# Kernel optimization log

Hardware: AMD Instinct MI355X
Metric: run time of the kernel (lower is better)

## Reference

```python
import jax, jax.numpy as jnp
import numpy as np

HEADS = 8
RANK = 4

def _lora(x, w_down, w_up, palette, in_dim, out_dim):
    # w_down: [RANK*in_dim, 15], w_up: [RANK*out_dim, 15], palette: [1, 15]
    down = (palette @ w_down.T).reshape(RANK, in_dim)   # [r, in]
    up = (palette @ w_up.T).reshape(out_dim, RANK)      # [out, r]
    return (x @ down.T) @ up.T                          # [..., out]


def setup_inputs() -> dict:
    key = jax.random.key(0)
    ks = jax.random.split(key, 16)
    B, S, D = 2, 2048, 1280
    def n(k, shape, std=0.02):
        return (jax.random.normal(k, shape, dtype=jnp.float32) * std).astype(jnp.float32)
    return {
        'hidden_states': jax.random.normal(ks[0], (B, S, D), dtype=jnp.float32),
        'color_palette': jax.random.uniform(ks[1], (1, 15), dtype=jnp.float32),
        'Wq': n(ks[2], (D, D)), 'Wk': n(ks[3], (D, D)),
        'Wv': n(ks[4], (D, D)), 'Wo': n(ks[5], (D, D)),
        'bo': jnp.zeros((D,), dtype=jnp.float32),
        'q_down': n(ks[6], (RANK * D, 15), 0.25), 'q_up': n(ks[7], (RANK * D, 15)),
        'k_down': n(ks[8], (RANK * D, 15), 0.25), 'k_up': n(ks[9], (RANK * D, 15)),
        'v_down': n(ks[10], (RANK * D, 15), 0.25), 'v_up': n(ks[11], (RANK * D, 15)),
        'o_down': n(ks[12], (RANK * D, 15), 0.25), 'o_up': n(ks[13], (RANK * D, 15)),
    }


def reference(hidden_states, color_palette, Wq, Wk, Wv, Wo, bo,
              q_down, q_up, k_down, k_up, v_down, v_up, o_down, o_up):
    B, S, D = hidden_states.shape
    H = HEADS
    hd = D // H
    scale = 1.0  # LoRA scale
    x = hidden_states
    # LoRA-augmented projections (self-attention: encoder_hidden_states = x)
    q = x @ Wq.T + scale * _lora(x, q_down, q_up, color_palette, D, D)
    k = x @ Wk.T + scale * _lora(x, k_down, k_up, color_palette, D, D)
    v = x @ Wv.T + scale * _lora(x, v_down, v_up, color_palette, D, D)
    # split heads: [B, S, D] -> [B, H, S, hd]
    q = q.reshape(B, S, H, hd).transpose(0, 2, 1, 3)
    k = k.reshape(B, S, H, hd).transpose(0, 2, 1, 3)
    v = v.reshape(B, S, H, hd).transpose(0, 2, 1, 3)
    attn_scale = 1.0 / jnp.sqrt(jnp.asarray(hd, dtype=q.dtype))
    scores = jnp.einsum('bhqd,bhkd->bhqk', q, k) * attn_scale
    probs = jax.nn.softmax(scores, axis=-1)
    out = jnp.einsum('bhqk,bhkd->bhqd', probs, v)
    out = out.transpose(0, 2, 1, 3).reshape(B, S, D)
    out = out @ Wo.T + bo + scale * _lora(out, o_down, o_up, color_palette, D, D)
    return out
```

## Files before the change

### kernel.cpp

```cpp
#include <hip/hip_runtime.h>

typedef unsigned short u16;
typedef unsigned int u32;
typedef __attribute__((ext_vector_type(4))) float floatx4;
typedef __attribute__((ext_vector_type(16))) float floatx16;
typedef __attribute__((ext_vector_type(8))) __bf16 bf16x8;
typedef __attribute__((ext_vector_type(2))) unsigned int u32x2;
typedef __attribute__((ext_vector_type(4))) unsigned int u32x4;

#define MFMA_BF16(a, b, c) __builtin_amdgcn_mfma_f32_16x16x32_bf16((a), (b), (c), 0, 0, 0)
#define MFMA32(a, b, c) __builtin_amdgcn_mfma_f32_32x32x16_bf16((a), (b), (c), 0, 0, 0)

typedef const __attribute__((address_space(1))) void* gas_ptr;
typedef __attribute__((address_space(3))) void* las_ptr;

__device__ __forceinline__ void gll16(const void* g, void* l) {
  __builtin_amdgcn_global_load_lds((gas_ptr)g, (las_ptr)l, 16, 0, 0);
}

__device__ __forceinline__ u16 f2bf(float x) {
  u32 u = __builtin_bit_cast(u32, x);
  u = (u + 0x7fffu + ((u >> 16) & 1u)) >> 16;
  return (u16)u;
}

__device__ __forceinline__ u32 cvtpk(float lo, float hi) {
  u32 r;
  asm("v_cvt_pk_bf16_f32 %0, %1, %2" : "=v"(r) : "v"(lo), "v"(hi));
  return r;
}

template <int WN>
__device__ __forceinline__ void vwait() {
  if constexpr (WN == 6) asm volatile("s_waitcnt vmcnt(6)" ::: "memory");
  else if constexpr (WN == 4) asm volatile("s_waitcnt vmcnt(4)" ::: "memory");
}

__global__ void prep_downup(const float* __restrict__ pal,
                            const float* __restrict__ qd, const float* __restrict__ qu,
                            const float* __restrict__ kd, const float* __restrict__ ku,
                            const float* __restrict__ vd, const float* __restrict__ vu,
                            const float* __restrict__ od, const float* __restrict__ ou,
                            float* __restrict__ down_f, float* __restrict__ up_f) {
  int tid = blockIdx.x * blockDim.x + threadIdx.x;
  int w = tid / 10240;
  int rem = tid - w * 10240;
  const float* dsrc = (w == 0) ? qd : (w == 1) ? kd : (w == 2) ? vd : od;
  const float* usrc = (w == 0) ? qu : (w == 1) ? ku : (w == 2) ? vu : ou;
  bool isdown = rem < 5120;
  int row = isdown ? rem : rem - 5120;
  const float* src = (isdown ? dsrc : usrc) + row * 15;
  float s = 0.f;
#pragma unroll
  for (int p = 0; p < 15; ++p) s += pal[p] * src[p];
  if (isdown) down_f[w * 5120 + row] = s;
  else        up_f[w * 5120 + row] = s;
}

__global__ void build_weff(const float* __restrict__ Wq, const float* __restrict__ Wk,
                           const float* __restrict__ Wv, const float* __restrict__ Wo,
                           const float* __restrict__ down_f, const float* __restrict__ up_f,
                           u16* __restrict__ weff_qkv, u16* __restrict__ weff_o) {
  int tid = blockIdx.x * blockDim.x + threadIdx.x;
  int w = tid / 1638400;
  int rem = tid - w * 1638400;
  int n = rem / 1280;
  int k = rem - n * 1280;
  const float* W = (w == 0) ? Wq : (w == 1) ? Wk : (w == 2) ? Wv : Wo;
  const float* up = up_f + w * 5120 + n * 4;
  const float* dn = down_f + w * 5120 + k;
  float v = W[rem] + up[0] * dn[0] + up[1] * dn[1280] + up[2] * dn[2560] + up[3] * dn[3840];
  u16 hv = f2bf(v);
  if (w < 3) weff_qkv[w * 1638400 + rem] = hv;
  else       weff_o[rem] = hv;
}

__global__ void cvt_x(const float4* __restrict__ x, ushort4* __restrict__ xb) {
  int i = blockIdx.x * blockDim.x + threadIdx.x;
  float4 v = x[i];
  ushort4 o;
  o.x = f2bf(v.x); o.y = f2bf(v.y); o.z = f2bf(v.z); o.w = f2bf(v.w);
  xb[i] = o;
}

__global__ __launch_bounds__(512) void gemm256_qkv(const u16* __restrict__ A, const u16* __restrict__ Bm,
                                                   u16* __restrict__ qb, u16* __restrict__ kb,
                                                   u16* __restrict__ vbuf, int K) {
  __shared__ __align__(16) u16 lA[2][16384];
  __shared__ __align__(16) u16 lB[2][16384];
  const int t = threadIdx.x;
  const int lane = t & 63;
  const int l15 = lane & 15, quad = lane >> 4;
  const int wid = t >> 6;
  const int wm = wid >> 2;
  const int wn = wid & 3;
  const int l = blockIdx.y * 16 + blockIdx.x;
  const int v = (l & 7) * 30 + (l >> 3);
  const int bm = (v & 15) * 256;
  const int bn = (v >> 4) * 256;
  floatx4 acc[8][4] = {};

  const int r0 = t >> 3, pos = t & 7;
  const long sof0 = (long)r0 * K + ((pos + r0) & 7) * 8;
  const long sof1 = (long)(r0 + 64) * K + ((pos + r0 + 64) & 7) * 8;

  int afo[4][2], bfo[2][2];
#pragma unroll
  for (int ch = 0; ch < 2; ++ch) {
    int kc8 = ch * 4 + quad;
#pragma unroll
    for (int mi = 0; mi < 4; ++mi) {
      int ra = wm * 128 + mi * 16 + l15;
      afo[mi][ch] = ra * 64 + ((kc8 - ra) & 7) * 8;
    }
#pragma unroll
    for (int ni = 0; ni < 2; ++ni) {
      int rb = wn * 64 + ni * 16 + l15;
      bfo[ni][ch] = rb * 64 + ((kc8 - rb) & 7) * 8;
    }
  }

  const u16* Ab = A + (long)bm * K;
  const u16* Bb = Bm + (long)bn * K;

#define PHASE(CB, Q, SB, SMAT, SH, ST, WN)                                           \
  {                                                                                   \
    const u16* gsrc = (SMAT) ? Bb : Ab;                                               \
    u16* ld0 = ((SMAT) ? &lB[SB][0] : &lA[SB][0]) + ((SH) * 1024 + t) * 8;            \
    gll16(gsrc + sof0 + (long)(SH) * 128 * K + (long)(ST) * 64, ld0);                 \
    gll16(gsrc + sof1 + (long)(SH) * 128 * K + (long)(ST) * 64, ld0 + 4096);          \
    vwait<WN>();                                                                      \
    __builtin_amdgcn_s_barrier();                                                     \
    __builtin_amdgcn_sched_barrier(0);                                                \
    constexpr int mh = (Q) >> 1, nh = (Q) & 1;                                        \
    bf16x8 af[4][2], bfr[2][2];                                                       \
    _Pragma("unroll") for (int ch = 0; ch < 2; ++ch) {                                \
      _Pragma("unroll") for (int mi = 0; mi < 4; ++mi)                                \
        af[mi][ch] = *(const bf16x8*)(&lA[CB][0] + afo[mi][ch] + mh * 4096);          \
      _Pragma("unroll") for (int ni = 0; ni < 2; ++ni)                                \
        bfr[ni][ch] = *(const bf16x8*)(&lB[CB][0] + bfo[ni][ch] + nh * 2048);         \
    }                                                                                 \
    asm volatile("s_waitcnt lgkmcnt(0)" ::: "memory");                                \
    __builtin_amdgcn_sched_barrier(0);                                                \
    __builtin_amdgcn_s_setprio(1);                                                    \
    _Pragma("unroll") for (int ch = 0; ch < 2; ++ch)                                  \
      _Pragma("unroll") for (int mi = 0; mi < 4; ++mi)                                \
        _Pragma("unroll") for (int ni = 0; ni < 2; ++ni)                              \
          acc[mh * 4 + mi][nh * 2 + ni] =                                             \
              MFMA_BF16(af[mi][ch], bfr[ni][ch], acc[mh * 4 + mi][nh * 2 + ni]);      \
    __builtin_amdgcn_s_setprio(0);                                                    \
  }

  gll16(Ab + sof0, &lA[0][t * 8]);
  gll16(Ab + sof1, &lA[0][t * 8 + 4096]);
  gll16(Bb + sof0, &lB[0][t * 8]);
  gll16(Bb + sof1, &lB[0][t * 8 + 4096]);
  gll16(Ab + sof0 + 128L * K, &lA[0][(1024 + t) * 8]);
  gll16(Ab + sof1 + 128L * K, &lA[0][(1024 + t) * 8 + 4096]);
  gll16(Bb + sof0 + 128L * K, &lB[0][(1024 + t) * 8]);
  gll16(Bb + sof1 + 128L * K, &lB[0][(1024 + t) * 8 + 4096]);

  const int niter = K >> 7;
  for (int i = 0; i < niter; ++i) {
    const int t1 = 2 * i + 1, t2 = 2 * i + 2;
    PHASE(0, 0, 1, 0, 0, t1, 6);
    PHASE(0, 1, 1, 1, 0, t1, 4);
    PHASE(0, 2, 1, 0, 1, t1, 0);
    PHASE(0, 3, 1, 1, 1, t1, 0);
    PHASE(1, 0, 0, 0, 0, t2, 6);
    PHASE(1, 1, 0, 1, 0, t2, 4);
    PHASE(1, 2, 0, 0, 1, t2, 0);
    PHASE(1, 3, 0, 1, 1, t2, 0);
  }
#undef PHASE
  asm volatile("s_waitcnt vmcnt(0)" ::: "memory");

#pragma unroll
  for (int mi8 = 0; mi8 < 8; ++mi8) {
#pragma unroll
    for (int ni4 = 0; ni4 < 4; ++ni4) {
#pragma unroll
      for (int r = 0; r < 4; ++r) {
        int m = bm + wm * 128 + (mi8 >> 2) * 64 + (mi8 & 3) * 16 + quad * 4 + r;
        int n = bn + wn * 64 + (ni4 >> 1) * 32 + (ni4 & 1) * 16 + l15;
        u16 hv = f2bf(acc[mi8][ni4][r]);
        if (n < 1280) {
          qb[(long)m * 1280 + n] = hv;
        } else if (n < 2560) {
          kb[(long)m * 1280 + (n - 1280)] = hv;
        } else {
          vbuf[(long)m * 1280 + (n - 2560)] = hv;
        }
      }
    }
  }
}

__global__ __launch_bounds__(256) void vtrans(const u16* __restrict__ vbuf,
                                              u16* __restrict__ vtb) {
  __shared__ u16 tile[64 * 65];
  const int t = threadIdx.x;
  const int sb = blockIdx.x * 64, nb = blockIdx.y * 64, b = blockIdx.z;
  const u16* src = vbuf + ((long)(b * 2048 + sb)) * 1280 + nb;
#pragma unroll
  for (int it = 0; it < 16; ++it) {
    int idx = t + it * 256;
    int s = idx >> 6, n = idx & 63;
    tile[s * 65 + n] = src[(long)s * 1280 + n];
  }
  __syncthreads();
  u16* dst = vtb + ((long)(b * 1280 + nb)) * 2048 + sb;
#pragma unroll
  for (int it = 0; it < 16; ++it) {
    int idx = t + it * 256;
    int n = idx >> 6, s = idx & 63;
    dst[(long)n * 2048 + s] = tile[s * 65 + n];
  }
}

__global__ __launch_bounds__(256) void gemm128_o(const u16* __restrict__ A, const u16* __restrict__ Bm,
                                                 float* __restrict__ outf,
                                                 const float* __restrict__ bias, int K) {
  __shared__ __align__(16) u16 lA[128 * 64];
  __shared__ __align__(16) u16 lB[128 * 64];
  const int t = threadIdx.x;
  const int lane = t & 63;
  const int l15 = lane & 15, quad = lane >> 4;
  const int wid = t >> 6;
  const int wm = (wid >> 1) * 64;
  const int wn = (wid & 1) * 64;
  const int bm = blockIdx.x * 128;
  const int bn = blockIdx.y * 128;
  floatx4 acc[4][4] = {};

  int soff[4];
#pragma unroll
  for (int i = 0; i < 4; ++i) {
    int c = t + i * 256;
    int row = c >> 3, pos = c & 7;
    soff[i] = row * K + ((pos + row) & 7) * 8;
  }
  int afo[4][2], bfo[4][2];
#pragma unroll
  for (int i = 0; i < 4; ++i) {
#pragma unroll
    for (int ch = 0; ch < 2; ++ch) {
      int ra = wm + i * 16 + l15;
      int rb = wn + i * 16 + l15;
      int kc8 = ch * 4 + quad;
      afo[i][ch] = ra * 64 + ((kc8 - ra) & 7) * 8;
      bfo[i][ch] = rb * 64 + ((kc8 - rb) & 7) * 8;
    }
  }

  const u16* Ab = A + (long)bm * K;
  const u16* Bb = Bm + (long)bn * K;
  const int nkt = K >> 6;

  for (int kt = 0; kt < nkt; ++kt) {
    __syncthreads();
    const int k0 = kt * 64;
#pragma unroll
    for (int i = 0; i < 4; ++i) gll16(Ab + (long)soff[i] + k0, lA + (t + i * 256) * 8);
#pragma unroll
    for (int i = 0; i < 4; ++i) gll16(Bb + (long)soff[i] + k0, lB + (t + i * 256) * 8);
    __syncthreads();
#pragma unroll
    for (int ch = 0; ch < 2; ++ch) {
      bf16x8 af[4], bfr[4];
#pragma unroll
      for (int i = 0; i < 4; ++i) af[i] = *(const bf16x8*)(lA + afo[i][ch]);
#pragma unroll
      for (int i = 0; i < 4; ++i) bfr[i] = *(const bf16x8*)(lB + bfo[i][ch]);
#pragma unroll
      for (int i = 0; i < 4; ++i)
#pragma unroll
        for (int j = 0; j < 4; ++j)
          acc[i][j] = MFMA_BF16(af[i], bfr[j], acc[i][j]);
    }
  }

#pragma unroll
  for (int i = 0; i < 4; ++i) {
#pragma unroll
    for (int j = 0; j < 4; ++j) {
#pragma unroll
      for (int r = 0; r < 4; ++r) {
        int m = bm + wm + i * 16 + quad * 4 + r;
        int n = bn + wn + j * 16 + l15;
        outf[(long)m * 1280 + n] = acc[i][j][r] + bias[n];
      }
    }
  }
}

__global__ __launch_bounds__(512) void flash_attn(const u16* __restrict__ qb,
                                                  const u16* __restrict__ kb,
                                                  const u16* __restrict__ vtb,
                                                  u16* __restrict__ attn) {
  const int D = 1280, HD = 160;
  __shared__ __align__(16) u16 kv_lds[2][20480];
  const int t = threadIdx.x, lane = t & 63, wid = t >> 6;
  const int l31 = lane & 31, hi = lane >> 5;
  const int rg = wid >> 1, kh = wid & 1;
  const int lflat = blockIdx.y * 16 + blockIdx.x;
  const int vswz = (lflat & 7) * 32 + (lflat >> 3);
  const int qi = vswz & 15, bh = vswz >> 4;
  const int b = bh >> 3, h = bh & 7;
  const int q0 = qi * 128 + rg * 32;
  const float kS = 0.11404582025f;

  bf16x8 aq[10];
  {
    const u16* qg = qb + ((long)(b * 2048 + q0 + l31)) * D + h * HD + hi * 8;
#pragma unroll
    for (int kw = 0; kw < 10; ++kw) aq[kw] = *(const bf16x8*)(qg + kw * 16);
  }

  const u16* sg[5];
  int sadv[5];
#pragma unroll
  for (int i = 0; i < 5; ++i) {
    int c = t + i * 512;
    if (c < 1280) {
      int key = c / 20, pos = c - key * 20;
      int g = pos - (3 * key) % 20;
      if (g < 0) g += 20;
      sg[i] = kb + ((long)(b * 2048 + key)) * D + h * HD + g * 8;
      sadv[i] = 64 * D;
    } else {
      int c2 = c - 1280;
      int vrow = c2 >> 3, swz = c2 & 7;
      int vcol = swz ^ (vrow & 7);
      sg[i] = vtb + ((long)(b * 1280 + h * HD + vrow)) * 2048 + vcol * 8;
      sadv[i] = 64;
    }
  }

  int kfo[10];
  {
    int key = kh * 32 + l31;
    int r3 = (3 * key) % 20;
#pragma unroll
    for (int kw = 0; kw < 10; ++kw) {
      int g = kw * 2 + hi;
      int pos = g + r3;
      if (pos >= 20) pos -= 20;
      kfo[kw] = (key * 20 + pos) * 8;
    }
  }
  int vfo[5][2];
#pragma unroll
  for (int db = 0; db < 5; ++db) {
#pragma unroll
    for (int w = 0; w < 2; ++w) {
      int d = db * 32 + l31;
      int gc = kh * 4 + w * 2 + hi;
      int sw = gc ^ (d & 7);
      vfo[db][w] = 10240 + (d * 8 + sw) * 8;
    }
  }

  float l_sum = 0.f;
  floatx16 o_acc[5] = {};
  bf16x8 paA = {}, paB = {};

  gll16(sg[0], &kv_lds[0][t * 8]);           sg[0] += sadv[0];
  gll16(sg[1], &kv_lds[0][(t + 512) * 8]);   sg[1] += sadv[1];
  if (wid < 4) { gll16(sg[2], &kv_lds[0][(t + 1024) * 8]); sg[2] += sadv[2]; }

  for (int kt0 = 0; kt0 < 32; ++kt0) {
    u16* kd = &kv_lds[(kt0 + 1) & 1][0];
    u16* vd = &kv_lds[kt0 & 1][0];
    if (kt0 < 31) {
      gll16(sg[0], kd + t * 8);          sg[0] += sadv[0];
      gll16(sg[1], kd + (t + 512) * 8);  sg[1] += sadv[1];
      if (wid < 4) { gll16(sg[2], kd + (t + 1024) * 8); sg[2] += sadv[2]; }
    }
    if (wid >= 4) { gll16(sg[2], vd + (t + 1024) * 8); sg[2] += sadv[2]; }
    gll16(sg[3], vd + (t + 1536) * 8);  sg[3] += sadv[3];
    gll16(sg[4], vd + (t + 2048) * 8);  sg[4] += sadv[4];

    if (kt0 < 31) asm volatile("s_waitcnt vmcnt(5)" ::: "memory");
    else          asm volatile("s_waitcnt vmcnt(0)" ::: "memory");
    __builtin_amdgcn_s_barrier();
    __builtin_amdgcn_sched_barrier(0);

    const u16* kbase = &kv_lds[kt0 & 1][0];
    const u16* vbase = &kv_lds[(kt0 + 1) & 1][0];

    floatx16 s0 = {}, s1 = {};
#pragma unroll
    for (int kw = 0; kw < 5; ++kw) {
      bf16x8 k0 = *(const bf16x8*)(kbase + kfo[kw * 2]);
      bf16x8 k1 = *(const bf16x8*)(kbase + kfo[kw * 2 + 1]);
      s0 = MFMA32(k0, aq[kw * 2], s0);
      s1 = MFMA32(k1, aq[kw * 2 + 1], s1);
    }

    if (kt0 > 0) {
#pragma unroll
      for (int db = 0; db < 5; ++db) {
        bf16x8 v0 = *(const bf16x8*)(vbase + vfo[db][0]);
        bf16x8 v1 = *(const bf16x8*)(vbase + vfo[db][1]);
        o_acc[db] = MFMA32(paA, v0, o_acc[db]);
        o_acc[db] = MFMA32(paB, v1, o_acc[db]);
      }
    }

    float p[16];
#pragma unroll
    for (int r = 0; r < 16; ++r) {
      p[r] = __builtin_exp2f(fminf((s0[r] + s1[r]) * kS, 80.f));
      l_sum += p[r];
    }
    u32 c01 = cvtpk(p[0], p[1]),  c23 = cvtpk(p[2], p[3]);
    u32 c45 = cvtpk(p[4], p[5]),  c67 = cvtpk(p[6], p[7]);
    u32 c89 = cvtpk(p[8], p[9]),  cAB = cvtpk(p[10], p[11]);
    u32 cCD = cvtpk(p[12], p[13]), cEF = cvtpk(p[14], p[15]);
    u32x2 r02 = __builtin_amdgcn_permlane32_swap(c01, c45, false, false);
    u32x2 r13 = __builtin_amdgcn_permlane32_swap(c23, c67, false, false);
    u32x2 r46 = __builtin_amdgcn_permlane32_swap(c89, cCD, false, false);
    u32x2 r57 = __builtin_amdgcn_permlane32_swap(cAB, cEF, false, false);
    u32x4 pk0 = {r02[0], r13[0], r02[1], r13[1]};
    u32x4 pk1 = {r46[0], r57[0], r46[1], r57[1]};
    paA = __builtin_bit_cast(bf16x8, pk0);
    paB = __builtin_bit_cast(bf16x8, pk1);

    __builtin_amdgcn_sched_barrier(0);
    __builtin_amdgcn_s_barrier();
  }

  {
    const u16* vbase = &kv_lds[1][0];
#pragma unroll
    for (int db = 0; db < 5; ++db) {
      bf16x8 v0 = *(const bf16x8*)(vbase + vfo[db][0]);
      bf16x8 v1 = *(const bf16x8*)(vbase + vfo[db][1]);
      o_acc[db] = MFMA32(paA, v0, o_acc[db]);
      o_acc[db] = MFMA32(paB, v1, o_acc[db]);
    }
  }
  __syncthreads();

  float* lscr = (float*)&kv_lds[0][0];
  lscr[wid * 64 + lane] = l_sum;
  __syncthreads();
  float rl[16];
#pragma unroll
  for (int r = 0; r < 16; ++r) {
    int q32 = (r & 3) + 8 * (r >> 2) + 4 * hi;
    float tot = lscr[(rg * 2 + 0) * 64 + q32] + lscr[(rg * 2 + 0) * 64 + q32 + 32]
              + lscr[(rg * 2 + 1) * 64 + q32] + lscr[(rg * 2 + 1) * 64 + q32 + 32];
    rl[r] = 1.0f / tot;
  }
  __syncthreads();
  float* oscr = (float*)&kv_lds[0][0];
  if (kh == 1) {
#pragma unroll
    for (int db = 0; db < 5; ++db)
#pragma unroll
      for (int r = 0; r < 16; ++r)
        oscr[rg * 5120 + (db * 16 + r) * 64 + lane] = o_acc[db][r];
  }
  __syncthreads();
  if (kh == 0) {
#pragma unroll
    for (int db = 0; db < 5; ++db) {
#pragma unroll
      for (int r = 0; r < 16; ++r) {
        float v = (o_acc[db][r] + oscr[rg * 5120 + (db * 16 + r) * 64 + lane]) * rl[r];
        int row = q0 + (r & 3) + 8 * (r >> 2) + 4 * hi;
        int col = h * HD + db * 32 + l31;
        attn[((long)(b * 2048 + row)) * D + col] = f2bf(v);
      }
    }
  }
}

extern "C" void kernel_launch(void* const* d_in, const int* in_sizes, int n_in,
                              void* d_out, int out_size, void* d_ws, size_t ws_size,
                              hipStream_t stream) {
  const float* x   = (const float*)d_in[0];
  const float* pal = (const float*)d_in[1];
  const float* Wq  = (const float*)d_in[2];
  const float* Wk  = (const float*)d_in[3];
  const float* Wv  = (const float*)d_in[4];
  const float* Wo  = (const float*)d_in[5];
  const float* bo  = (const float*)d_in[6];
  const float* qd  = (const float*)d_in[7];
  const float* qu  = (const float*)d_in[8];
  const float* kd  = (const float*)d_in[9];
  const float* ku  = (const float*)d_in[10];
  const float* vd  = (const float*)d_in[11];
  const float* vu  = (const float*)d_in[12];
  const float* od  = (const float*)d_in[13];
  const float* ou  = (const float*)d_in[14];
  float* out = (float*)d_out;

  char* ws = (char*)d_ws;
  u16* xb       = (u16*)(ws);
  u16* weff_qkv = (u16*)(ws + 10485760);
  u16* weff_o   = (u16*)(ws + 20316160);
  u16* qbuf     = (u16*)(ws + 23592960);
  u16* kbuf     = (u16*)(ws + 34078720);
  u16* vtb      = (u16*)(ws + 44564480);
  u16* attn     = (u16*)(ws + 55050240);
  float* down_f = (float*)(ws + 65536000);
  float* up_f   = (float*)(ws + 65617920);
  u16* vbuf     = (u16*)(ws + 65699840);

  prep_downup<<<160, 256, 0, stream>>>(pal, qd, qu, kd, ku, vd, vu, od, ou, down_f, up_f);
  build_weff<<<25600, 256, 0, stream>>>(Wq, Wk, Wv, Wo, down_f, up_f, weff_qkv, weff_o);
  cvt_x<<<5120, 256, 0, stream>>>((const float4*)x, (ushort4*)xb);
  gemm256_qkv<<<dim3(16, 15), 512, 0, stream>>>(xb, weff_qkv, qbuf, kbuf, vbuf, 1280);
  vtrans<<<dim3(32, 20, 2), 256, 0, stream>>>(vbuf, vtb);
  flash_attn<<<dim3(16, 16), 512, 0, stream>>>(qbuf, kbuf, vtb, attn);
  gemm128_o<<<dim3(32, 10), 256, 0, stream>>>(attn, weff_o, out, bo, 1280);
}
```

Measured before the change: 267.5 us.

## Fuse V transpose into QKV GEMM epilogue and merge weight build with x conversion

Replaces the 256x256 multi-phase pipelined QKV GEMM with a simpler 128x128 single-buffered GEMM. For V tiles it transposes the result through shared memory and writes the transposed V directly, which removes the separate vtrans kernel and the intermediate vbuf round trip. It also merges the cvt_x kernel into build_weff as extra blocks, saving one launch. The cost is that the new GEMM drops the double-buffered, barrier-interleaved pipeline and does one load-then-compute sync per k-step, which may lower MFMA utilisation.

```diff
diff --git a/kernel.cpp b/kernel.cpp
--- a/kernel.cpp
+++ b/kernel.cpp
@@ -28,12 +28,6 @@
   u32 r;
   asm("v_cvt_pk_bf16_f32 %0, %1, %2" : "=v"(r) : "v"(lo), "v"(hi));
   return r;
-}
-
-template <int WN>
-__device__ __forceinline__ void vwait() {
-  if constexpr (WN == 6) asm volatile("s_waitcnt vmcnt(6)" ::: "memory");
-  else if constexpr (WN == 4) asm volatile("s_waitcnt vmcnt(4)" ::: "memory");
 }
 
 __global__ void prep_downup(const float* __restrict__ pal,
@@ -57,10 +51,19 @@
   else        up_f[w * 5120 + row] = s;
 }
 
-__global__ void build_weff(const float* __restrict__ Wq, const float* __restrict__ Wk,
-                           const float* __restrict__ Wv, const float* __restrict__ Wo,
-                           const float* __restrict__ down_f, const float* __restrict__ up_f,
-                           u16* __restrict__ weff_qkv, u16* __restrict__ weff_o) {
+__global__ void build_weff_cvtx(const float* __restrict__ Wq, const float* __restrict__ Wk,
+                                const float* __restrict__ Wv, const float* __restrict__ Wo,
+                                const float* __restrict__ down_f, const float* __restrict__ up_f,
+                                u16* __restrict__ weff_qkv, u16* __restrict__ weff_o,
+                                const float4* __restrict__ x, ushort4* __restrict__ xb) {
+  if (blockIdx.x >= 25600) {
+    int i = (blockIdx.x - 25600) * blockDim.x + threadIdx.x;
+    float4 v = x[i];
+    ushort4 o;
+    o.x = f2bf(v.x); o.y = f2bf(v.y); o.z = f2bf(v.z); o.w = f2bf(v.w);
+    xb[i] = o;
+    return;
+  }
   int tid = blockIdx.x * blockDim.x + threadIdx.x;
   int w = tid / 1638400;
   int rem = tid - w * 1638400;
@@ -75,146 +78,107 @@
   else       weff_o[rem] = hv;
 }
 
-__global__ void cvt_x(const float4* __restrict__ x, ushort4* __restrict__ xb) {
-  int i = blockIdx.x * blockDim.x + threadIdx.x;
-  float4 v = x[i];
-  ushort4 o;
-  o.x = f2bf(v.x); o.y = f2bf(v.y); o.z = f2bf(v.z); o.w = f2bf(v.w);
-  xb[i] = o;
-}
-
-__global__ __launch_bounds__(512) void gemm256_qkv(const u16* __restrict__ A, const u16* __restrict__ Bm,
+__global__ __launch_bounds__(256) void gemm128_qkv(const u16* __restrict__ A, const u16* __restrict__ Bm,
                                                    u16* __restrict__ qb, u16* __restrict__ kb,
-                                                   u16* __restrict__ vbuf, int K) {
-  __shared__ __align__(16) u16 lA[2][16384];
-  __shared__ __align__(16) u16 lB[2][16384];
+                                                   u16* __restrict__ vtb, int K) {
+  __shared__ __align__(16) u16 smem[128 * 136];
+  u16* lA = smem;
+  u16* lB = smem + 8192;
   const int t = threadIdx.x;
   const int lane = t & 63;
   const int l15 = lane & 15, quad = lane >> 4;
   const int wid = t >> 6;
-  const int wm = wid >> 2;
-  const int wn = wid & 3;
-  const int l = blockIdx.y * 16 + blockIdx.x;
-  const int v = (l & 7) * 30 + (l >> 3);
-  const int bm = (v & 15) * 256;
-  const int bn = (v >> 4) * 256;
-  floatx4 acc[8][4] = {};
-
-  const int r0 = t >> 3, pos = t & 7;
-  const long sof0 = (long)r0 * K + ((pos + r0) & 7) * 8;
-  const long sof1 = (long)(r0 + 64) * K + ((pos + r0 + 64) & 7) * 8;
-
-  int afo[4][2], bfo[2][2];
-#pragma unroll
-  for (int ch = 0; ch < 2; ++ch) {
-    int kc8 = ch * 4 + quad;
-#pragma unroll
-    for (int mi = 0; mi < 4; ++mi) {
-      int ra = wm * 128 + mi * 16 + l15;
-      afo[mi][ch] = ra * 64 + ((kc8 - ra) & 7) * 8;
-    }
-#pragma unroll
-    for (int ni = 0; ni < 2; ++ni) {
-      int rb = wn * 64 + ni * 16 + l15;
-      bfo[ni][ch] = rb * 64 + ((kc8 - rb) & 7) * 8;
+  const int wm = (wid >> 1) * 64;
+  const int wn = (wid & 1) * 64;
+  const int bm = blockIdx.x * 128;
+  const int bn = blockIdx.y * 128;
+  floatx4 acc[4][4] = {};
+
+  int soff[4];
+#pragma unroll
+  for (int i = 0; i < 4; ++i) {
+    int c = t + i * 256;
+    int row = c >> 3, pos = c & 7;
+    soff[i] = row * K + ((pos + row) & 7) * 8;
+  }
+  int afo[4][2], bfo[4][2];
+#pragma unroll
+  for (int i = 0; i < 4; ++i) {
+#pragma unroll
+    for (int ch = 0; ch < 2; ++ch) {
+      int ra = wm + i * 16 + l15;
+      int rb = wn + i * 16 + l15;
+      int kc8 = ch * 4 + quad;
+      afo[i][ch] = ra * 64 + ((kc8 - ra) & 7) * 8;
+      bfo[i][ch] = rb * 64 + ((kc8 - rb) & 7) * 8;
     }
   }
 
   const u16* Ab = A + (long)bm * K;
   const u16* Bb = Bm + (long)bn * K;
-
-#define PHASE(CB, Q, SB, SMAT, SH, ST, WN)                                           \
-  {                                                                                   \
-    const u16* gsrc = (SMAT) ? Bb : Ab;                                               \
-    u16* ld0 = ((SMAT) ? &lB[SB][0] : &lA[SB][0]) + ((SH) * 1024 + t) * 8;            \
-    gll16(gsrc + sof0 + (long)(SH) * 128 * K + (long)(ST) * 64, ld0);                 \
-    gll16(gsrc + sof1 + (long)(SH) * 128 * K + (long)(ST) * 64, ld0 + 4096);          \
-    vwait<WN>();                                                                      \
-    __builtin_amdgcn_s_barrier();                                                     \
-    __builtin_amdgcn_sched_barrier(0);                                                \
-    constexpr int mh = (Q) >> 1, nh = (Q) & 1;                                        \
-    bf16x8 af[4][2], bfr[2][2];                                                       \
-    _Pragma("unroll") for (int ch = 0; ch < 2; ++ch) {                                \
-      _Pragma("unroll") for (int mi = 0; mi < 4; ++mi)                                \
-        af[mi][ch] = *(const bf16x8*)(&lA[CB][0] + afo[mi][ch] + mh * 4096);          \
-      _Pragma("unroll") for (int ni = 0; ni < 2; ++ni)                                \
-        bfr[ni][ch] = *(const bf16x8*)(&lB[CB][0] + bfo[ni][ch] + nh * 2048);         \
-    }                                                                                 \
-    asm volatile("s_waitcnt lgkmcnt(0)" ::: "memory");                                \
-    __builtin_amdgcn_sched_barrier(0);                                                \
-    __builtin_amdgcn_s_setprio(1);                                                    \
-    _Pragma("unroll") for (int ch = 0; ch < 2; ++ch)                                  \
-      _Pragma("unroll") for (int mi = 0; mi < 4; ++mi)                                \
-        _Pragma("unroll") for (int ni = 0; ni < 2; ++ni)                              \
-          acc[mh * 4 + mi][nh * 2 + ni] =                                             \
-              MFMA_BF16(af[mi][ch], bfr[ni][ch], acc[mh * 4 + mi][nh * 2 + ni]);      \
-    __builtin_amdgcn_s_setprio(0);                                                    \
-  }
-
-  gll16(Ab + sof0, &lA[0][t * 8]);
-  gll16(Ab + sof1, &lA[0][t * 8 + 4096]);
-  gll16(Bb + sof0, &lB[0][t * 8]);
-  gll16(Bb + sof1, &lB[0][t * 8 + 4096]);
-  gll16(Ab + sof0 + 128L * K, &lA[0][(1024 + t) * 8]);
-  gll16(Ab + sof1 + 128L * K, &lA[0][(1024 + t) * 8 + 4096]);
-  gll16(Bb + sof0 + 128L * K, &lB[0][(1024 + t) * 8]);
-  gll16(Bb + sof1 + 128L * K, &lB[0][(1024 + t) * 8 + 4096]);
-
-  const int niter = K >> 7;
-  for (int i = 0; i < niter; ++i) {
-    const int t1 = 2 * i + 1, t2 = 2 * i + 2;
-    PHASE(0, 0, 1, 0, 0, t1, 6);
-    PHASE(0, 1, 1, 1, 0, t1, 4);
-    PHASE(0, 2, 1, 0, 1, t1, 0);
-    PHASE(0, 3, 1, 1, 1, t1, 0);
-    PHASE(1, 0, 0, 0, 0, t2, 6);
-    PHASE(1, 1, 0, 1, 0, t2, 4);
-    PHASE(1, 2, 0, 0, 1, t2, 0);
-    PHASE(1, 3, 0, 1, 1, t2, 0);
-  }
-#undef PHASE
-  asm volatile("s_waitcnt vmcnt(0)" ::: "memory");
-
-#pragma unroll
-  for (int mi8 = 0; mi8 < 8; ++mi8) {
-#pragma unroll
-    for (int ni4 = 0; ni4 < 4; ++ni4) {
-#pragma unroll
-      for (int r = 0; r < 4; ++r) {
-        int m = bm + wm * 128 + (mi8 >> 2) * 64 + (mi8 & 3) * 16 + quad * 4 + r;
-        int n = bn + wn * 64 + (ni4 >> 1) * 32 + (ni4 & 1) * 16 + l15;
-        u16 hv = f2bf(acc[mi8][ni4][r]);
-        if (n < 1280) {
-          qb[(long)m * 1280 + n] = hv;
-        } else if (n < 2560) {
-          kb[(long)m * 1280 + (n - 1280)] = hv;
-        } else {
-          vbuf[(long)m * 1280 + (n - 2560)] = hv;
+  const int nkt = K >> 6;
+
+  for (int kt = 0; kt < nkt; ++kt) {
+    __syncthreads();
+    const int k0 = kt * 64;
+#pragma unroll
+    for (int i = 0; i < 4; ++i) gll16(Ab + (long)soff[i] + k0, lA + (t + i * 256) * 8);
+#pragma unroll
+    for (int i = 0; i < 4; ++i) gll16(Bb + (long)soff[i] + k0, lB + (t + i * 256) * 8);
+    __syncthreads();
+#pragma unroll
+    for (int ch = 0; ch < 2; ++ch) {
+      bf16x8 af[4], bfr[4];
+#pragma unroll
+      for (int i = 0; i < 4; ++i) af[i] = *(const bf16x8*)(lA + afo[i][ch]);
+#pragma unroll
+      for (int i = 0; i < 4; ++i) bfr[i] = *(const bf16x8*)(lB + bfo[i][ch]);
+#pragma unroll
+      for (int i = 0; i < 4; ++i)
+#pragma unroll
+        for (int j = 0; j < 4; ++j)
+          acc[i][j] = MFMA_BF16(af[i], bfr[j], acc[i][j]);
+    }
+  }
+
+  if (bn < 2560) {
+#pragma unroll
+    for (int i = 0; i < 4; ++i) {
+#pragma unroll
+      for (int j = 0; j < 4; ++j) {
+#pragma unroll
+        for (int r = 0; r < 4; ++r) {
+          int m = bm + wm + i * 16 + quad * 4 + r;
+          int n = bn + wn + j * 16 + l15;
+          u16 hv = f2bf(acc[i][j][r]);
+          if (n < 1280) qb[(long)m * 1280 + n] = hv;
+          else          kb[(long)m * 1280 + (n - 1280)] = hv;
         }
       }
     }
-  }
-}
-
-__global__ __launch_bounds__(256) void vtrans(const u16* __restrict__ vbuf,
-                                              u16* __restrict__ vtb) {
-  __shared__ u16 tile[64 * 65];
-  const int t = threadIdx.x;
-  const int sb = blockIdx.x * 64, nb = blockIdx.y * 64, b = blockIdx.z;
-  const u16* src = vbuf + ((long)(b * 2048 + sb)) * 1280 + nb;
-#pragma unroll
-  for (int it = 0; it < 16; ++it) {
-    int idx = t + it * 256;
-    int s = idx >> 6, n = idx & 63;
-    tile[s * 65 + n] = src[(long)s * 1280 + n];
-  }
-  __syncthreads();
-  u16* dst = vtb + ((long)(b * 1280 + nb)) * 2048 + sb;
-#pragma unroll
-  for (int it = 0; it < 16; ++it) {
-    int idx = t + it * 256;
-    int n = idx >> 6, s = idx & 63;
-    dst[(long)n * 2048 + s] = tile[s * 65 + n];
+  } else {
+    __syncthreads();
+#pragma unroll
+    for (int i = 0; i < 4; ++i)
+#pragma unroll
+      for (int j = 0; j < 4; ++j)
+#pragma unroll
+        for (int r = 0; r < 4; ++r) {
+          int m_loc = wm + i * 16 + quad * 4 + r;
+          int n_loc = wn + j * 16 + l15;
+          smem[n_loc * 136 + m_loc] = f2bf(acc[i][j][r]);
+        }
+    __syncthreads();
+    const int b = bm >> 11, sbase = bm & 2047;
+    u16* dst = vtb + ((long)(b * 1280 + (bn - 2560))) * 2048 + sbase;
+#pragma unroll
+    for (int it = 0; it < 8; ++it) {
+      int idx = it * 256 + t;
+      int n_loc = idx >> 4;
+      int m0 = (idx & 15) * 8;
+      bf16x8 vv = *(const bf16x8*)(smem + n_loc * 136 + m0);
+      *(bf16x8*)(dst + (long)n_loc * 2048 + m0) = vv;
+    }
   }
 }
 
@@ -508,13 +472,11 @@
   u16* attn     = (u16*)(ws + 55050240);
   float* down_f = (float*)(ws + 65536000);
   float* up_f   = (float*)(ws + 65617920);
-  u16* vbuf     = (u16*)(ws + 65699840);
 
   prep_downup<<<160, 256, 0, stream>>>(pal, qd, qu, kd, ku, vd, vu, od, ou, down_f, up_f);
-  build_weff<<<25600, 256, 0, stream>>>(Wq, Wk, Wv, Wo, down_f, up_f, weff_qkv, weff_o);
-  cvt_x<<<5120, 256, 0, stream>>>((const float4*)x, (ushort4*)xb);
-  gemm256_qkv<<<dim3(16, 15), 512, 0, stream>>>(xb, weff_qkv, qbuf, kbuf, vbuf, 1280);
-  vtrans<<<dim3(32, 20, 2), 256, 0, stream>>>(vbuf, vtb);
+  build_weff_cvtx<<<30720, 256, 0, stream>>>(Wq, Wk, Wv, Wo, down_f, up_f, weff_qkv, weff_o,
+                                             (const float4*)x, (ushort4*)xb);
+  gemm128_qkv<<<dim3(32, 30), 256, 0, stream>>>(xb, weff_qkv, qbuf, kbuf, vtb, 1280);
   flash_attn<<<dim3(16, 16), 512, 0, stream>>>(qbuf, kbuf, vtb, attn);
   gemm128_o<<<dim3(32, 10), 256, 0, stream>>>(attn, weff_o, out, bo, 1280);
 }
```

Measured after the change: 267.6 us. Within noise of the previous version (+0.0%).
